# Optimization experiments

Hardware: AMD Instinct MI355X
Metric: run time of the kernel (lower is better)

The kernel has to match this reference:

```python
import jax, jax.numpy as jnp
import numpy as np

KERNELS = (4, 4, 8, 8, 8, 16, 16)
HEADS = (4, 4, 8, 8, 8, 16, 16)
PATCH = 2
EPS = 1e-5


def _layer_norm(x, w, b):
    mu = jnp.mean(x, axis=-1, keepdims=True)
    var = jnp.mean(jnp.square(x - mu), axis=-1, keepdims=True)
    return (x - mu) * jax.lax.rsqrt(var + EPS) * w + b


def _sliding_kernel_attention(x, w_qkv, k, heads):
    # x: (B, H, W, C) channels-last. Unfold -> per-window attention over the
    # k*k pixels (token dim = C) -> overlap-add fold (stride 1).
    B, H, W, C = x.shape
    Lh, Lw = H - k + 1, W - k + 1
    scale = (C // heads) ** -0.5
    ih = jnp.arange(Lh)[:, None] + jnp.arange(k)[None, :]   # (Lh, k)
    iw = jnp.arange(Lw)[:, None] + jnp.arange(k)[None, :]   # (Lw, k)
    pat = x[:, ih][:, :, :, iw]                             # (B, Lh, k, Lw, k, C)
    tok = pat.transpose(0, 1, 3, 2, 4, 5).reshape(B, Lh * Lw, k * k, C)
    qkv = jnp.einsum('blnc,dc->blnd', tok, w_qkv)           # (B, L, k*k, 3C)
    q, kk, v = jnp.split(qkv, 3, axis=-1)
    attn = jax.nn.softmax(jnp.einsum('blqc,blkc->blqk', q, kk) * scale, axis=-1)
    o = jnp.einsum('blqk,blkc->blqc', attn, v)              # (B, L, k*k, C)
    o = o.reshape(B, Lh, Lw, k, k, C).transpose(0, 1, 3, 2, 4, 5)  # (B,Lh,k,Lw,k,C)
    # overlap-add fold back to (B, H, W, C); duplicate indices accumulate
    return jnp.zeros_like(x).at[:, ih[:, :, None, None], iw[None, None, :, :], :].add(o)


def _block(x, ln1_w, ln1_b, w_qkv, ln2_w, ln2_b, w1, b1, w2, b2, k, heads):
    x = x + _sliding_kernel_attention(_layer_norm(x, ln1_w, ln1_b), w_qkv, k, heads)
    h = _layer_norm(x, ln2_w, ln2_b)
    h = jax.nn.gelu(h @ w1.T + b1, approximate=False)
    return x + (h @ w2.T + b2)


def _forward(x, patch_w, patch_b, row_emb, col_emb, cls_tok, ln1_w, ln1_b, qkv_w,
             ln2_w, ln2_b, mlp_w1, mlp_b1, mlp_w2, mlp_b2, cls_w, cls_b):
    # patch embed: conv k=stride=PATCH; output laid out channels-last (B, G, G, C)
    h = jax.lax.conv_general_dilated(
        x, patch_w, (PATCH, PATCH), 'VALID',
        dimension_numbers=('NCHW', 'OIHW', 'NHWC')) + patch_b
    B, G, _, C = h.shape
    # 2D positional embedding: row half + col half concatenated on channels
    pos = jnp.concatenate([
        jnp.broadcast_to(row_emb[:, None, :], (G, G, C // 2)),
        jnp.broadcast_to(col_emb[None, :, :], (G, G, C // 2))], axis=-1)
    h = h + pos
    # cls token: one extra row prepended along H (torch cat on dim=2)
    cls = jnp.broadcast_to(cls_tok, (B, 1, G, C))
    h = jnp.concatenate([cls, h], axis=1)                   # (B, G+1, G, C)
    for i in range(7):
        h = _block(h, ln1_w[i], ln1_b[i], qkv_w[i], ln2_w[i], ln2_b[i],
                   mlp_w1[i], mlp_b1[i], mlp_w2[i], mlp_b2[i],
                   KERNELS[i], HEADS[i])
    return h[:, 0, 0, :] @ cls_w.T + cls_b                  # (B, num_classes)


def setup_inputs() -> dict:
    key = jax.random.key(0)
    ks = jax.random.split(key, 8)
    B, C, G, NCLS, NB = 16, 256, 16, 1000, 7
    s = 0.02
    return {
        'x': jax.random.normal(ks[0], (B, 3, 32, 32), jnp.float32),
        'patch_w': jax.random.normal(ks[1], (C, 3, PATCH, PATCH), jnp.float32) * s,
        'patch_b': jnp.zeros((C,), jnp.float32),
        'row_emb': jax.random.normal(ks[2], (G, C // 2), jnp.float32) * s,
        'col_emb': jax.random.normal(ks[3], (G, C // 2), jnp.float32) * s,
        'cls_tok': jnp.zeros((C,), jnp.float32),
        'ln1_w': jnp.ones((NB, C), jnp.float32),
        'ln1_b': jnp.zeros((NB, C), jnp.float32),
        'qkv_w': jax.random.normal(ks[4], (NB, 3 * C, C), jnp.float32) * s,
        'ln2_w': jnp.ones((NB, C), jnp.float32),
        'ln2_b': jnp.zeros((NB, C), jnp.float32),
        'mlp_w1': jax.random.normal(ks[5], (NB, 2 * C, C), jnp.float32) * s,
        'mlp_b1': jnp.zeros((NB, 2 * C), jnp.float32),
        'mlp_w2': jax.random.normal(ks[6], (NB, C, 2 * C), jnp.float32) * s,
        'mlp_b2': jnp.zeros((NB, C), jnp.float32),
        'cls_w': jax.random.normal(ks[7], (NCLS, C), jnp.float32) * s,
        'cls_b': jnp.zeros((NCLS,), jnp.float32),
    }


def reference(x, patch_w, patch_b, row_emb, col_emb, cls_tok, ln1_w, ln1_b, qkv_w,
              ln2_w, ln2_b, mlp_w1, mlp_b1, mlp_w2, mlp_b2, cls_w, cls_b):
    return _forward(x, patch_w, patch_b, row_emb, col_emb, cls_tok, ln1_w, ln1_b,
                    qkv_w, ln2_w, ln2_b, mlp_w1, mlp_b1, mlp_w2, mlp_b2, cls_w, cls_b)
```

## Files before the change

kernel.cpp:

```cpp
#include <hip/hip_runtime.h>
#include <cmath>

#define NPIX 4352
#define C_DIM 256

typedef unsigned short ushort_t;
typedef unsigned int uint_t;
typedef float f32x4 __attribute__((ext_vector_type(4)));
typedef __bf16 bfx8 __attribute__((ext_vector_type(8)));

__device__ __forceinline__ ushort_t f2bf(float f) {
    uint_t u = __float_as_uint(f);
    u = (u + 0x7FFFu + ((u >> 16) & 1u)) >> 16;
    return (ushort_t)u;
}
__device__ __forceinline__ float bf2f(ushort_t b) {
    return __uint_as_float(((uint_t)b) << 16);
}
__device__ __forceinline__ float gelu_f(float v) {
    return 0.5f * v * (1.0f + erff(v * 0.70710678118654752f));
}

__global__ __launch_bounds__(256) void conv3_bf16(
    const float* __restrict__ a, ushort_t* __restrict__ oa, int na,
    const float* __restrict__ b, ushort_t* __restrict__ ob, int nb,
    const float* __restrict__ c, ushort_t* __restrict__ oc, int nc)
{
    int ntot = na + nb + nc;
    for (int i = blockIdx.x * 256 + threadIdx.x; i < ntot; i += gridDim.x * 256) {
        if (i < na)            oa[i] = f2bf(a[i]);
        else if (i < na + nb)  ob[i - na] = f2bf(b[i - na]);
        else                   oc[i - na - nb] = f2bf(c[i - na - nb]);
    }
}

__global__ __launch_bounds__(256) void patch_embed_ln(
    const float* __restrict__ x, const float* __restrict__ pw,
    const float* __restrict__ pb, const float* __restrict__ row_emb,
    const float* __restrict__ col_emb, const float* __restrict__ cls_tok,
    const float* __restrict__ lw, const float* __restrict__ lb,
    float* __restrict__ out, ushort_t* __restrict__ lnout)
{
    __shared__ float red[8];
    int p = blockIdx.x;
    int c = threadIdx.x;
    int b = p / 272;
    int rem = p - b * 272;
    int y = rem >> 4;
    int xw = rem & 15;
    float v;
    if (y == 0) {
        v = cls_tok[c];
    } else {
        int gr = y - 1, gc = xw;
        const float* xb = x + (size_t)b * 3 * 1024;
        const float* wc = pw + (size_t)c * 12;
        float acc = pb[c];
        #pragma unroll
        for (int ci = 0; ci < 3; ci++)
            #pragma unroll
            for (int ph = 0; ph < 2; ph++)
                #pragma unroll
                for (int pq = 0; pq < 2; pq++)
                    acc += xb[ci * 1024 + (2 * gr + ph) * 32 + (2 * gc + pq)]
                         * wc[(ci * 2 + ph) * 2 + pq];
        acc += (c < 128) ? row_emb[gr * 128 + c] : col_emb[gc * 128 + (c - 128)];
        v = acc;
    }
    out[(size_t)p * C_DIM + c] = v;
    float s = v;
    s += __shfl_down(s, 32); s += __shfl_down(s, 16); s += __shfl_down(s, 8);
    s += __shfl_down(s, 4);  s += __shfl_down(s, 2);  s += __shfl_down(s, 1);
    if ((c & 63) == 0) red[c >> 6] = s;
    __syncthreads();
    float mu = (red[0] + red[1] + red[2] + red[3]) * (1.0f / 256.0f);
    float d = v - mu;
    float s2 = d * d;
    s2 += __shfl_down(s2, 32); s2 += __shfl_down(s2, 16); s2 += __shfl_down(s2, 8);
    s2 += __shfl_down(s2, 4);  s2 += __shfl_down(s2, 2);  s2 += __shfl_down(s2, 1);
    if ((c & 63) == 0) red[4 + (c >> 6)] = s2;
    __syncthreads();
    float var = (red[4] + red[5] + red[6] + red[7]) * (1.0f / 256.0f);
    lnout[(size_t)p * C_DIM + c] = f2bf(d * rsqrtf(var + 1e-5f) * lw[c] + lb[c]);
}

__global__ __launch_bounds__(256) void layernorm_k(
    const float* __restrict__ in, const float* __restrict__ w,
    const float* __restrict__ b, ushort_t* __restrict__ out)
{
    __shared__ float red[8];
    int r = blockIdx.x, c = threadIdx.x;
    float v = in[(size_t)r * C_DIM + c];
    float s = v;
    s += __shfl_down(s, 32); s += __shfl_down(s, 16); s += __shfl_down(s, 8);
    s += __shfl_down(s, 4);  s += __shfl_down(s, 2);  s += __shfl_down(s, 1);
    if ((c & 63) == 0) red[c >> 6] = s;
    __syncthreads();
    float mu = (red[0] + red[1] + red[2] + red[3]) * (1.0f / 256.0f);
    float d = v - mu;
    float s2 = d * d;
    s2 += __shfl_down(s2, 32); s2 += __shfl_down(s2, 16); s2 += __shfl_down(s2, 8);
    s2 += __shfl_down(s2, 4);  s2 += __shfl_down(s2, 2);  s2 += __shfl_down(s2, 1);
    if ((c & 63) == 0) red[4 + (c >> 6)] = s2;
    __syncthreads();
    float var = (red[4] + red[5] + red[6] + red[7]) * (1.0f / 256.0f);
    out[(size_t)r * C_DIM + c] = f2bf(d * rsqrtf(var + 1e-5f) * w[c] + b[c]);
}

template <int BM, int BN, int MODE>
__global__ __launch_bounds__(256) void gemm_v2(
    const ushort_t* __restrict__ A, const ushort_t* __restrict__ B,
    const float* __restrict__ bias, const float* __restrict__ res,
    void* __restrict__ outp, ushort_t* __restrict__ vT, int K, int ldo)
{
    constexpr int MI = BM / 32, NJ = BN / 32;
    constexpr int AG = BM * 4, BG = BN * 4;
    constexpr int AU = AG / 256, BU = BG / 256;
    constexpr int HALF = (BM + BN) * 32;
    constexpr int STAGE_E = 2 * HALF;
    constexpr int BOUNCE_E = BM * (BN + 8);
    constexpr int SMEM_E = (STAGE_E > BOUNCE_E) ? STAGE_E : BOUNCE_E;
    __shared__ ushort_t sm[SMEM_E];

    int m0 = blockIdx.x * BM, n0 = blockIdx.y * BN;
    int t = threadIdx.x, lane = t & 63, wv = t >> 6;
    int l15 = lane & 15, lg = lane >> 4;
    int wr = wv >> 1, wc = wv & 1;

    const int nt = K / 32;
    f32x4 acc[MI][NJ] = {};
    uint4 ra[AU], rb[BU];

    #pragma unroll
    for (int u = 0; u < AU; u++) {
        int g = t + u * 256, row = g >> 2, p = g & 3;
        int ps = p ^ ((row >> 1) & 3);
        ra[u] = *(const uint4*)(A + (size_t)(m0 + row) * K + ps * 8);
    }
    #pragma unroll
    for (int u = 0; u < BU; u++) {
        int g = t + u * 256, col = g >> 2, p = g & 3;
        int ps = p ^ ((col >> 1) & 3);
        rb[u] = *(const uint4*)(B + (size_t)(n0 + col) * K + ps * 8);
    }
    #pragma unroll
    for (int u = 0; u < AU; u++) *(uint4*)(sm + (t + u * 256) * 8) = ra[u];
    #pragma unroll
    for (int u = 0; u < BU; u++) *(uint4*)(sm + BM * 32 + (t + u * 256) * 8) = rb[u];
    __syncthreads();

    for (int ks = 0; ks < nt; ks++) {
        int coff = (ks & 1) * HALF, noff = ((ks & 1) ^ 1) * HALF;
        if (ks + 1 < nt) {
            int k1 = (ks + 1) * 32;
            #pragma unroll
            for (int u = 0; u < AU; u++) {
                int g = t + u * 256, row = g >> 2, p = g & 3;
                int ps = p ^ ((row >> 1) & 3);
                ra[u] = *(const uint4*)(A + (size_t)(m0 + row) * K + k1 + ps * 8);
            }
            #pragma unroll
            for (int u = 0; u < BU; u++) {
                int g = t + u * 256, col = g >> 2, p = g & 3;
                int ps = p ^ ((col >> 1) & 3);
                rb[u] = *(const uint4*)(B + (size_t)(n0 + col) * K + k1 + ps * 8);
            }
        }
        bfx8 af[MI], bf[NJ];
        #pragma unroll
        for (int i = 0; i < MI; i++) {
            int row = wr * (BM / 2) + i * 16 + l15;
            af[i] = *(const bfx8*)(sm + coff + row * 32 + ((lg ^ ((row >> 1) & 3)) << 3));
        }
        #pragma unroll
        for (int j = 0; j < NJ; j++) {
            int col = wc * (BN / 2) + j * 16 + l15;
            bf[j] = *(const bfx8*)(sm + coff + BM * 32 + col * 32 + ((lg ^ ((col >> 1) & 3)) << 3));
        }
        #pragma unroll
        for (int i = 0; i < MI; i++)
            #pragma unroll
            for (int j = 0; j < NJ; j++)
                acc[i][j] = __builtin_amdgcn_mfma_f32_16x16x32_bf16(af[i], bf[j], acc[i][j], 0, 0, 0);
        if (ks + 1 < nt) {
            #pragma unroll
            for (int u = 0; u < AU; u++) *(uint4*)(sm + noff + (t + u * 256) * 8) = ra[u];
            #pragma unroll
            for (int u = 0; u < BU; u++) *(uint4*)(sm + noff + BM * 32 + (t + u * 256) * 8) = rb[u];
        }
        __syncthreads();
    }

    if (MODE == 0 && n0 >= 512) {
        #pragma unroll
        for (int i = 0; i < MI; i++) {
            int mb = m0 + wr * (BM / 2) + i * 16 + lg * 4;
            #pragma unroll
            for (int j = 0; j < NJ; j++) {
                int nv = n0 - 512 + wc * (BN / 2) + j * 16 + l15;
                ushort4 pk;
                pk.x = f2bf(acc[i][j][0]); pk.y = f2bf(acc[i][j][1]);
                pk.z = f2bf(acc[i][j][2]); pk.w = f2bf(acc[i][j][3]);
                *(ushort4*)&vT[(size_t)nv * NPIX + mb] = pk;
            }
        }
        return;
    }
    if (MODE == 3) {
        float* o = (float*)outp;
        #pragma unroll
        for (int i = 0; i < MI; i++) {
            #pragma unroll
            for (int j = 0; j < NJ; j++) {
                int col = n0 + wc * (BN / 2) + j * 16 + l15;
                float bz = bias[col];
                #pragma unroll
                for (int r = 0; r < 4; r++) {
                    int row = m0 + wr * (BM / 2) + i * 16 + lg * 4 + r;
                    o[(size_t)row * ldo + col] = acc[i][j][r] + bz + res[(size_t)row * ldo + col];
                }
            }
        }
        return;
    }
    __syncthreads();
    #pragma unroll
    for (int i = 0; i < MI; i++) {
        #pragma unroll
        for (int j = 0; j < NJ; j++) {
            int cl = wc * (BN / 2) + j * 16 + l15;
            float bz = (MODE == 2) ? bias[n0 + cl] : 0.0f;
            #pragma unroll
            for (int r = 0; r < 4; r++) {
                int rl = wr * (BM / 2) + i * 16 + lg * 4 + r;
                float v = acc[i][j][r];
                if (MODE == 2) v = gelu_f(v + bz);
                sm[rl * (BN + 8) + cl] = f2bf(v);
            }
        }
    }
    __syncthreads();
    ushort_t* ob = (ushort_t*)outp;
    #pragma unroll
    for (int e = 0; e < BM * BN; e += 2048) {
        int idx = e + t * 8;
        int rl = idx / BN, cl = idx % BN;
        uint4 v = *(const uint4*)(sm + rl * (BN + 8) + cl);
        *(uint4*)&ob[(size_t)(m0 + rl) * ldo + n0 + cl] = v;
    }
}

__device__ __forceinline__ uint2 ld_u4_align(const uint_t* drow, int e0) {
    int d0 = e0 >> 1;
    if (!(e0 & 1)) return make_uint2(drow[d0], drow[d0 + 1]);
    uint_t a = drow[d0], b = drow[d0 + 1], c = drow[d0 + 2];
    return make_uint2((a >> 16) | (b << 16), (b >> 16) | (c << 16));
}
__device__ __forceinline__ uint4 ld_u8_align(const uint_t* drow, int e0) {
    int d0 = e0 >> 1;
    if (!(e0 & 1)) return make_uint4(drow[d0], drow[d0 + 1], drow[d0 + 2], drow[d0 + 3]);
    uint_t a = drow[d0], b = drow[d0 + 1], c = drow[d0 + 2], d = drow[d0 + 3], e = drow[d0 + 4];
    return make_uint4((a >> 16) | (b << 16), (b >> 16) | (c << 16),
                      (c >> 16) | (d << 16), (d >> 16) | (e << 16));
}

template <int KK>
__global__ __launch_bounds__(256) void attn_v2(
    const ushort_t* __restrict__ qk, const ushort_t* __restrict__ vT,
    ushort_t* __restrict__ obuf, int w0, int nW, float scale)
{
    constexpr int T = KK * KK;
    constexpr int Lh = 18 - KK, Lw = 17 - KK, L = Lh * Lw;
    constexpr int NF   = 1;
    constexpr int NJ   = 8;
    constexpr int PSTR = 40;
    constexpr int KROWS = 32;
    constexpr int VROWS = 256;
    constexpr int EOFF = 2048;
    constexpr int ESTR = 128;

    __shared__ ushort_t Klds[KROWS * 256];
    __shared__ ushort_t Vlds[VROWS * 64];
    __shared__ ushort_t Plds[4][16 * PSTR];

    int t = threadIdx.x, lane = t & 63, wv = t >> 6;
    int l15 = lane & 15, lg = lane >> 4;

    int wrel = blockIdx.x * 2 + (wv & 1);
    int wloc = wv & 1, chalf = wv >> 1, qbase = 0;
    if (wrel >= nW) wrel = nW - 1;

    int pbs[2];
    #pragma unroll
    for (int w = 0; w < 2; w++) {
        int wi = blockIdx.x * 2 + w;
        if (wi >= nW) wi = nW - 1;
        wi += w0;
        int b = wi / L, lrem = wi % L;
        pbs[w] = b * 272 + (lrem / Lw) * 16 + (lrem % Lw);
    }

    int qtok = qbase + l15;
    int qpix = pbs[wloc] + ((qtok >> 2) << 4) + (qtok & 3);
    bfx8 qf[8];
    #pragma unroll
    for (int cs = 0; cs < 8; cs++)
        qf[cs] = *(const bfx8*)(qk + (size_t)qpix * 512 + cs * 32 + lg * 8);

    f32x4 o[NJ] = {};
    float lsum[4] = {0.f, 0.f, 0.f, 0.f};

    for (int g = t; g < KROWS * 32; g += 256) {
        int row = g >> 5, cg = g & 31;
        int pix = pbs[row >> 4] + (((row & 15) >> 2) << 4) + (row & 3);
        uint4 v = *(const uint4*)(qk + (size_t)pix * 512 + 256 + cg * 8);
        *(uint4*)(Klds + row * 256 + ((cg ^ (row & 7)) << 3)) = v;
    }
    for (int g = t; g < VROWS * 8; g += 256) {
        int cr = g >> 3, c16 = g & 7;
        const uint_t* drow = (const uint_t*)(vT + (size_t)cr * NPIX);
        uint4 v;
        int w = c16 >> 2, sub = c16 & 3;
        if (sub < 2) {
            int pix0 = pbs[w] + (sub << 5);
            uint2 a  = ld_u4_align(drow, pix0);
            uint2 b2 = ld_u4_align(drow, pix0 + 16);
            v = make_uint4(a.x, a.y, b2.x, b2.y);
        } else v = make_uint4(0, 0, 0, 0);
        *(uint4*)(Vlds + cr * 64 + ((c16 ^ (cr & 7)) << 3)) = v;
    }
    __syncthreads();
    f32x4 s[NF];
    #pragma unroll
    for (int j = 0; j < NF; j++) s[j] = f32x4{0.f, 0.f, 0.f, 0.f};
    #pragma unroll
    for (int cs = 0; cs < 8; cs++) {
        int krow = (wloc << 4) + l15;
        bfx8 kf = *(const bfx8*)(Klds + krow * 256 + ((((cs << 2) + lg) ^ (krow & 7)) << 3));
        s[0] = __builtin_amdgcn_mfma_f32_16x16x32_bf16(qf[cs], kf, s[0], 0, 0, 0);
    }
    float p[NF][4];
    #pragma unroll
    for (int r = 0; r < 4; r++) {
        float mx = s[0][r];
        mx = fmaxf(mx, __shfl_xor(mx, 1));
        mx = fmaxf(mx, __shfl_xor(mx, 2));
        mx = fmaxf(mx, __shfl_xor(mx, 4));
        mx = fmaxf(mx, __shfl_xor(mx, 8));
        float ps = 0.f;
        p[0][r] = __expf(scale * (s[0][r] - mx));
        ps += p[0][r];
        ps += __shfl_xor(ps, 1);
        ps += __shfl_xor(ps, 2);
        ps += __shfl_xor(ps, 4);
        ps += __shfl_xor(ps, 8);
        lsum[r] = ps;
    }
    ushort_t* Pw = Plds[wv];
    #pragma unroll
    for (int r = 0; r < 4; r++) {
        Pw[(lg * 4 + r) * PSTR + l15] = f2bf(p[0][r]);
        Pw[(lg * 4 + r) * PSTR + 16 + l15] = 0;
    }
    asm volatile("s_waitcnt lgkmcnt(0)" ::: "memory");
    __builtin_amdgcn_sched_barrier(0);
    {
        bfx8 pf = *(const bfx8*)(Pw + l15 * PSTR + (lg << 3));
        #pragma unroll
        for (int j = 0; j < NJ; j++) {
            int cr = chalf * 128 + (j << 4) + l15;
            int c16 = ((wloc << 2) + lg) ^ (cr & 7);
            bfx8 vf = *(const bfx8*)(Vlds + cr * 64 + (c16 << 3));
            o[j] = __builtin_amdgcn_mfma_f32_16x16x32_bf16(pf, vf, o[j], 0, 0, 0);
        }
    }
    asm volatile("s_waitcnt lgkmcnt(0)" ::: "memory");
    __syncthreads();
    float inv[4];
    #pragma unroll
    for (int r = 0; r < 4; r++) inv[r] = 1.0f / lsum[r];
    ushort_t* Ep = Klds + wv * EOFF;
    #pragma unroll
    for (int j = 0; j < NJ; j++)
        #pragma unroll
        for (int r = 0; r < 4; r++)
            Ep[(lg * 4 + r) * ESTR + (j << 4) + l15] = f2bf(o[j][r] * inv[r]);
    asm volatile("s_waitcnt lgkmcnt(0)" ::: "memory");
    __builtin_amdgcn_sched_barrier(0);
    size_t gb = ((size_t)wrel * T + qbase) * C_DIM + chalf * 128;
    #pragma unroll
    for (int i = 0; i < 4; i++) {
        int off = i * 512 + lane * 8;
        int row = off >> 7, col = off & 127;
        uint4 v = *(const uint4*)(Ep + row * ESTR + col);
        *(uint4*)(obuf + gb + (size_t)row * C_DIM + col) = v;
    }
}

__global__ __launch_bounds__(256) void attn_v3(
    const ushort_t* __restrict__ qk, const ushort_t* __restrict__ vT,
    ushort_t* __restrict__ obuf, int w0, float scale)
{
    __shared__ ushort_t SH[32768];
    const int Lw = 9, L = 90;
    int t = threadIdx.x, lane = t & 63, wv = t >> 6;
    int l15 = lane & 15, lg = lane >> 4;
    int wrel = blockIdx.x;
    int widx = w0 + wrel;
    int b = widx / L, lrem = widx % L;
    int pbase = b * 272 + (lrem / Lw) * 16 + (lrem % Lw);
    int qbase = wv * 16;

    int qtok = qbase + l15;
    int qpix = pbase + ((qtok >> 3) << 4) + (qtok & 7);
    bfx8 qf[8];
    #pragma unroll
    for (int cs = 0; cs < 8; cs++)
        qf[cs] = *(const bfx8*)(qk + (size_t)qpix * 512 + cs * 32 + lg * 8);

    for (int g = t; g < 64 * 32; g += 256) {
        int row = g >> 5, cg = g & 31;
        int pix = pbase + ((row >> 3) << 4) + (row & 7);
        uint4 v = *(const uint4*)(qk + (size_t)pix * 512 + 256 + cg * 8);
        *(uint4*)(SH + row * 256 + ((cg ^ (row & 7)) << 3)) = v;
    }
    for (int g = t; g < 256 * 8; g += 256) {
        int cr = g >> 3, c16 = g & 7;
        const uint_t* drow = (const uint_t*)(vT + (size_t)cr * NPIX);
        uint4 v = ld_u8_align(drow, pbase + (c16 << 4));
        *(uint4*)(SH + 16384 + cr * 64 + ((c16 ^ (cr & 7)) << 3)) = v;
    }
    __syncthreads();

    f32x4 s[4];
    #pragma unroll
    for (int j = 0; j < 4; j++) s[j] = f32x4{0.f, 0.f, 0.f, 0.f};
    #pragma unroll
    for (int cs = 0; cs < 8; cs++) {
        #pragma unroll
        for (int j = 0; j < 4; j++) {
            int krow = (j << 4) + l15;
            bfx8 kf = *(const bfx8*)(SH + krow * 256 + ((((cs << 2) + lg) ^ (krow & 7)) << 3));
            s[j] = __builtin_amdgcn_mfma_f32_16x16x32_bf16(qf[cs], kf, s[j], 0, 0, 0);
        }
    }
    float p[4][4], lsum[4];
    #pragma unroll
    for (int r = 0; r < 4; r++) {
        float mx = s[0][r];
        #pragma unroll
        for (int j = 1; j < 4; j++) mx = fmaxf(mx, s[j][r]);
        mx = fmaxf(mx, __shfl_xor(mx, 1));
        mx = fmaxf(mx, __shfl_xor(mx, 2));
        mx = fmaxf(mx, __shfl_xor(mx, 4));
        mx = fmaxf(mx, __shfl_xor(mx, 8));
        float ps = 0.f;
        #pragma unroll
        for (int j = 0; j < 4; j++) {
            p[j][r] = __expf(scale * (s[j][r] - mx));
            ps += p[j][r];
        }
        ps += __shfl_xor(ps, 1);
        ps += __shfl_xor(ps, 2);
        ps += __shfl_xor(ps, 4);
        ps += __shfl_xor(ps, 8);
        lsum[r] = ps;
    }
    __syncthreads();
    ushort_t* Pw = SH + wv * 1088;
    #pragma unroll
    for (int j = 0; j < 4; j++)
        #pragma unroll
        for (int r = 0; r < 4; r++)
            Pw[(lg * 4 + r) * 68 + (j << 4) + l15] = f2bf(p[j][r]);
    asm volatile("s_waitcnt lgkmcnt(0)" ::: "memory");
    __builtin_amdgcn_sched_barrier(0);
    f32x4 o[16] = {};
    #pragma unroll
    for (int kt = 0; kt < 2; kt++) {
        bfx8 pf = *(const bfx8*)(Pw + l15 * 68 + (kt << 5) + (lg << 3));
        #pragma unroll
        for (int j = 0; j < 16; j++) {
            int cr = (j << 4) + l15;
            int c16 = ((kt << 2) + lg) ^ (cr & 7);
            bfx8 vf = *(const bfx8*)(SH + 16384 + cr * 64 + (c16 << 3));
            o[j] = __builtin_amdgcn_mfma_f32_16x16x32_bf16(pf, vf, o[j], 0, 0, 0);
        }
    }
    asm volatile("s_waitcnt lgkmcnt(0)" ::: "memory");
    __syncthreads();
    float inv[4];
    #pragma unroll
    for (int r = 0; r < 4; r++) inv[r] = 1.0f / lsum[r];
    ushort_t* Ep = SH + wv * 4224;
    #pragma unroll
    for (int j = 0; j < 16; j++)
        #pragma unroll
        for (int r = 0; r < 4; r++)
            Ep[(lg * 4 + r) * 260 + (j << 4) + l15] = f2bf(o[j][r] * inv[r]);
    asm volatile("s_waitcnt lgkmcnt(0)" ::: "memory");
    __builtin_amdgcn_sched_barrier(0);
    size_t gb = ((size_t)wrel * 64 + qbase) * C_DIM;
    #pragma unroll
    for (int i = 0; i < 8; i++) {
        int off = i * 512 + lane * 8;
        int row = off >> 8, col = off & 255;
        uint4 v = *(const uint4*)(Ep + row * 260 + col);
        *(uint4*)(obuf + gb + off) = v;
    }
}

template <int PASS>
__global__ __launch_bounds__(256) void gemm_seq(
    const ushort_t* __restrict__ A, const ushort_t* __restrict__ B,
    const float* __restrict__ linv, void* __restrict__ outp)
{
    __shared__ ushort_t sm[8192];
    int m0 = blockIdx.x * 64, n0 = blockIdx.y * 64;
    int seq = blockIdx.z;
    int pbase = (seq >> 1) * 272 + (seq & 1) * 16;
    int t = threadIdx.x, lane = t & 63, wv = t >> 6;
    int l15 = lane & 15, lg = lane >> 4;
    int wr = wv >> 1, wc = wv & 1;

    f32x4 acc[2][2] = {};
    uint4 ra, rb;

    int g_row = t >> 2, g_p = t & 3;
    int g_ps = g_p ^ ((g_row >> 1) & 3);

    const ushort_t* Asrc;
    const ushort_t* Bsrc;
    if (PASS == 0) {
        Asrc = A + (size_t)(pbase + m0 + g_row) * 512 + g_ps * 8;
        Bsrc = B + (size_t)(pbase + n0 + g_row) * 512 + 256 + g_ps * 8;
    } else {
        Asrc = A + (size_t)seq * 65536 + (size_t)(m0 + g_row) * 256 + g_ps * 8;
        Bsrc = B + (size_t)(n0 + g_row) * NPIX + pbase + g_ps * 8;
    }

    ra = *(const uint4*)(Asrc);
    rb = *(const uint4*)(Bsrc);
    *(uint4*)(sm + t * 8) = ra;
    *(uint4*)(sm + 2048 + t * 8) = rb;
    __syncthreads();

    for (int ks = 0; ks < 8; ks++) {
        int coff = (ks & 1) * 4096, noff = ((ks & 1) ^ 1) * 4096;
        if (ks + 1 < 8) {
            int k1 = (ks + 1) * 32;
            ra = *(const uint4*)(Asrc + k1);
            rb = *(const uint4*)(Bsrc + k1);
        }
        bfx8 af[2], bf[2];
        #pragma unroll
        for (int i = 0; i < 2; i++) {
            int row = wr * 32 + i * 16 + l15;
            af[i] = *(const bfx8*)(sm + coff + row * 32 + ((lg ^ ((row >> 1) & 3)) << 3));
        }
        #pragma unroll
        for (int j = 0; j < 2; j++) {
            int col = wc * 32 + j * 16 + l15;
            bf[j] = *(const bfx8*)(sm + coff + 2048 + col * 32 + ((lg ^ ((col >> 1) & 3)) << 3));
        }
        #pragma unroll
        for (int i = 0; i < 2; i++)
            #pragma unroll
            for (int j = 0; j < 2; j++)
                acc[i][j] = __builtin_amdgcn_mfma_f32_16x16x32_bf16(af[i], bf[j], acc[i][j], 0, 0, 0);
        if (ks + 1 < 8) {
            *(uint4*)(sm + noff + t * 8) = ra;
            *(uint4*)(sm + noff + 2048 + t * 8) = rb;
        }
        __syncthreads();
    }

    if (PASS == 0) {
        float* S = (float*)outp + (size_t)seq * 65536;
        #pragma unroll
        for (int i = 0; i < 2; i++) {
            #pragma unroll
            for (int j = 0; j < 2; j++) {
                int col = n0 + wc * 32 + j * 16 + l15;
                #pragma unroll
                for (int r = 0; r < 4; r++) {
                    int row = m0 + wr * 32 + i * 16 + lg * 4 + r;
                    S[(size_t)row * 256 + col] = acc[i][j][r];
                }
            }
        }
        return;
    }
    ushort_t* ob = (ushort_t*)outp;
    #pragma unroll
    for (int i = 0; i < 2; i++) {
        #pragma unroll
        for (int j = 0; j < 2; j++) {
            int cl = wc * 32 + j * 16 + l15;
            #pragma unroll
            for (int r = 0; r < 4; r++) {
                int rl = wr * 32 + i * 16 + lg * 4 + r;
                float v = acc[i][j][r] * linv[seq * 256 + m0 + rl];
                sm[rl * 72 + cl] = f2bf(v);
            }
        }
    }
    __syncthreads();
    #pragma unroll
    for (int e = 0; e < 4096; e += 2048) {
        int idx = e + t * 8;
        int rl = idx >> 6, cl = idx & 63;
        uint4 v = *(const uint4*)(sm + rl * 72 + cl);
        *(uint4*)&ob[(size_t)seq * 65536 + (size_t)(m0 + rl) * 256 + n0 + cl] = v;
    }
}

__global__ __launch_bounds__(256) void rowsm(
    const float* __restrict__ sbuf, ushort_t* __restrict__ pbuf,
    float* __restrict__ linv, float scale)
{
    __shared__ float red[8];
    int r = blockIdx.x, t = threadIdx.x;
    float s = sbuf[(size_t)r * 256 + t];
    float m = s;
    m = fmaxf(m, __shfl_down(m, 32)); m = fmaxf(m, __shfl_down(m, 16));
    m = fmaxf(m, __shfl_down(m, 8));  m = fmaxf(m, __shfl_down(m, 4));
    m = fmaxf(m, __shfl_down(m, 2));  m = fmaxf(m, __shfl_down(m, 1));
    if ((t & 63) == 0) red[t >> 6] = m;
    __syncthreads();
    m = fmaxf(fmaxf(red[0], red[1]), fmaxf(red[2], red[3]));
    float p = __expf(scale * (s - m));
    float ps = p;
    ps += __shfl_down(ps, 32); ps += __shfl_down(ps, 16); ps += __shfl_down(ps, 8);
    ps += __shfl_down(ps, 4);  ps += __shfl_down(ps, 2);  ps += __shfl_down(ps, 1);
    if ((t & 63) == 0) red[4 + (t >> 6)] = ps;
    __syncthreads();
    float sum = red[4] + red[5] + red[6] + red[7];
    pbuf[(size_t)r * 256 + t] = f2bf(p);
    if (t == 0) linv[r] = 1.0f / sum;
}

__global__ __launch_bounds__(256) void fold_ln(
    const ushort_t* __restrict__ obuf, const float* __restrict__ xin,
    float* __restrict__ y, const float* __restrict__ lw,
    const float* __restrict__ lb, ushort_t* __restrict__ lnout, int do_ln,
    int k, int Lh, int Lw, int w0, int w1)
{
    __shared__ float red[8];
    int p = blockIdx.x;
    int c = threadIdx.x;
    int b = p / 272;
    int rem = p - b * 272;
    int yy = rem >> 4, xx = rem & 15;
    int L = Lh * Lw;
    int T = k * k;
    float acc = xin ? xin[(size_t)p * C_DIM + c] : y[(size_t)p * C_DIM + c];
    int lh0 = max(0, yy - k + 1), lh1 = min(Lh - 1, yy);
    int lw0 = max(0, xx - k + 1), lw1 = min(Lw - 1, xx);
    for (int lh = lh0; lh <= lh1; lh++) {
        for (int lw = lw0; lw <= lw1; lw++) {
            int widx = b * L + lh * Lw + lw;
            if (widx < w0 || widx >= w1) continue;
            int n = (yy - lh) * k + (xx - lw);
            acc += bf2f(obuf[((size_t)(widx - w0) * T + n) * C_DIM + c]);
        }
    }
    y[(size_t)p * C_DIM + c] = acc;
    if (!do_ln) return;
    float s = acc;
    s += __shfl_down(s, 32); s += __shfl_down(s, 16); s += __shfl_down(s, 8);
    s += __shfl_down(s, 4);  s += __shfl_down(s, 2);  s += __shfl_down(s, 1);
    if ((c & 63) == 0) red[c >> 6] = s;
    __syncthreads();
    float mu = (red[0] + red[1] + red[2] + red[3]) * (1.0f / 256.0f);
    float d = acc - mu;
    float s2 = d * d;
    s2 += __shfl_down(s2, 32); s2 += __shfl_down(s2, 16); s2 += __shfl_down(s2, 8);
    s2 += __shfl_down(s2, 4);  s2 += __shfl_down(s2, 2);  s2 += __shfl_down(s2, 1);
    if ((c & 63) == 0) red[4 + (c >> 6)] = s2;
    __syncthreads();
    float var = (red[4] + red[5] + red[6] + red[7]) * (1.0f / 256.0f);
    lnout[(size_t)p * C_DIM + c] = f2bf(d * rsqrtf(var + 1e-5f) * lw[c] + lb[c]);
}

__global__ __launch_bounds__(256) void classifier_k(
    const float* __restrict__ h, const float* __restrict__ cw,
    const float* __restrict__ cb, float* __restrict__ out)
{
    __shared__ float hrow[256];
    int b = blockIdx.x;
    int n = blockIdx.y * 256 + threadIdx.x;
    hrow[threadIdx.x] = h[(size_t)b * 272 * C_DIM + threadIdx.x];
    __syncthreads();
    if (n < 1000) {
        float acc = cb[n];
        const float* wr = cw + (size_t)n * C_DIM;
        for (int c = 0; c < 256; c++) acc += hrow[c] * wr[c];
        out[(size_t)b * 1000 + n] = acc;
    }
}

extern "C" void kernel_launch(void* const* d_in, const int* in_sizes, int n_in,
                              void* d_out, int out_size, void* d_ws, size_t ws_size,
                              hipStream_t stream)
{
    const float* x       = (const float*)d_in[0];
    const float* patch_w = (const float*)d_in[1];
    const float* patch_b = (const float*)d_in[2];
    const float* row_emb = (const float*)d_in[3];
    const float* col_emb = (const float*)d_in[4];
    const float* cls_tok = (const float*)d_in[5];
    const float* ln1_w   = (const float*)d_in[6];
    const float* ln1_b   = (const float*)d_in[7];
    const float* qkv_w   = (const float*)d_in[8];
    const float* ln2_w   = (const float*)d_in[9];
    const float* ln2_b   = (const float*)d_in[10];
    const float* mlp_w1  = (const float*)d_in[11];
    const float* mlp_b1  = (const float*)d_in[12];
    const float* mlp_w2  = (const float*)d_in[13];
    const float* mlp_b2  = (const float*)d_in[14];
    const float* cls_w   = (const float*)d_in[15];
    const float* cls_b   = (const float*)d_in[16];
    float* out = (float*)d_out;

    float* xb0  = (float*)d_ws;
    float* xb1  = xb0 + (size_t)NPIX * 256;
    ushort_t* lnb = (ushort_t*)(xb1 + (size_t)NPIX * 256);
    ushort_t* qkb = lnb + (size_t)NPIX * 256;
    ushort_t* vT  = qkb + (size_t)NPIX * 512;
    ushort_t* h1  = vT + (size_t)256 * NPIX;
    ushort_t* wq  = h1 + (size_t)NPIX * 512;
    ushort_t* w1b = wq + (size_t)7 * 768 * 256;
    ushort_t* w2b = w1b + (size_t)7 * 512 * 256;
    float* sbuf   = (float*)(w2b + (size_t)7 * 256 * 512);
    ushort_t* pbuf = (ushort_t*)(sbuf + (size_t)32 * 65536);
    float* linv   = (float*)(pbuf + (size_t)32 * 65536);
    ushort_t* obuf = (ushort_t*)(linv + 8192);
    size_t obuf_off_bytes = (size_t)((char*)obuf - (char*)d_ws);
    size_t obuf_cap_e = (ws_size > obuf_off_bytes + 64)
                        ? (ws_size - obuf_off_bytes - 64) / 2 : 0;

    conv3_bf16<<<1024, 256, 0, stream>>>(qkv_w, wq, 7 * 768 * 256,
                                         mlp_w1, w1b, 7 * 512 * 256,
                                         mlp_w2, w2b, 7 * 256 * 512);

    patch_embed_ln<<<NPIX, 256, 0, stream>>>(x, patch_w, patch_b, row_emb,
                                             col_emb, cls_tok, ln1_w, ln1_b,
                                             xb0, lnb);

    const int KS[7] = {4, 4, 8, 8, 8, 16, 16};
    float* xcur = xb0;
    float* ybuf = xb1;

    for (int i = 0; i < 7; i++) {
        int k = KS[i];
        int Lh = 18 - k, Lw = 17 - k, L = Lh * Lw, T = k * k;
        float scale = 1.0f / std::sqrt((float)(256 / k));

        if (i > 0)
            layernorm_k<<<NPIX, 256, 0, stream>>>(xcur, ln1_w + i * 256,
                                                  ln1_b + i * 256, lnb);
        gemm_v2<128, 128, 0><<<dim3(NPIX / 128, 6), 256, 0, stream>>>(
            lnb, wq + (size_t)i * 768 * 256, nullptr, nullptr, qkb, vT, 256, 512);

        if (k == 16) {
            gemm_seq<0><<<dim3(4, 4, 32), 256, 0, stream>>>(qkb, qkb, nullptr, sbuf);
            rowsm<<<8192, 256, 0, stream>>>(sbuf, pbuf, linv, scale);
            gemm_seq<1><<<dim3(4, 4, 32), 256, 0, stream>>>(pbuf, vT, linv, obuf);
            fold_ln<<<NPIX, 256, 0, stream>>>(obuf, xcur, ybuf,
                                              ln2_w + i * 256, ln2_b + i * 256,
                                              lnb, 1, k, Lh, Lw, 0, 32);
        } else {
            int totalW = 16 * L;
            size_t perW = (size_t)T * C_DIM;
            int maxW = (int)((obuf_cap_e / perW) < (size_t)totalW
                             ? (obuf_cap_e / perW) : (size_t)totalW);
            if (maxW < 2) maxW = 2;
            if (k == 4) maxW &= ~1;
            for (int w0 = 0; w0 < totalW; w0 += maxW) {
                int nW = totalW - w0 < maxW ? totalW - w0 : maxW;
                if (k == 4)
                    attn_v2<4><<<(nW + 1) / 2, 256, 0, stream>>>(qkb, vT, obuf, w0, nW, scale);
                else
                    attn_v3<<<nW, 256, 0, stream>>>(qkb, vT, obuf, w0, scale);
                int last = (w0 + nW >= totalW);
                fold_ln<<<NPIX, 256, 0, stream>>>(obuf, (w0 == 0) ? xcur : nullptr,
                                                  ybuf, ln2_w + i * 256, ln2_b + i * 256,
                                                  lnb, last, k, Lh, Lw, w0, w0 + nW);
            }
        }

        gemm_v2<64, 128, 2><<<dim3(NPIX / 64, 4), 256, 0, stream>>>(
            lnb, w1b + (size_t)i * 512 * 256, mlp_b1 + i * 512, nullptr, h1, nullptr, 256, 512);
        gemm_v2<64, 64, 3><<<dim3(NPIX / 64, 4), 256, 0, stream>>>(
            h1, w2b + (size_t)i * 256 * 512, mlp_b2 + i * 256, ybuf, xcur, nullptr, 512, 256);
    }

    classifier_k<<<dim3(16, 4), 256, 0, stream>>>(xcur, cls_w, cls_b, out);
}
```

Before: 725.6 us.

## Split overlap-add fold into row-sum and column-sum passes for small kernels

For k=4 and k=8 layers, when the whole attention output fits in the workspace, attention runs in a single launch instead of chunked windows. The fold then runs in two stages: foldA sums each window row's outputs along the horizontal direction into per-row partial sums, and foldB adds the vertical contributions, the residual and the layer norm. This replaces the per-pixel gather over k*k overlapping windows with separable summation, cutting redundant bf16 reads and removing the chunk loop. The cost is an extra fp32 rowsum buffer that shares space with sbuf, and obuf moves to a fixed offset after it.

Result: faster. 644.2 us (-11.2%).

```diff
diff --git a/kernel.cpp b/kernel.cpp
--- a/kernel.cpp
+++ b/kernel.cpp
@@ -638,6 +638,66 @@
     float sum = red[4] + red[5] + red[6] + red[7];
     pbuf[(size_t)r * 256 + t] = f2bf(p);
     if (t == 0) linv[r] = 1.0f / sum;
+}
+
+template <int K>
+__global__ __launch_bounds__(256) void foldA(
+    const ushort_t* __restrict__ obuf, float* __restrict__ rowsum)
+{
+    constexpr int Lh = 18 - K, Lw = 17 - K, L = Lh * Lw, T = K * K;
+    int c = threadIdx.x;
+    int bid = blockIdx.x;
+    int dy = bid % K;
+    int blh = bid / K;
+    int lh = blh % Lh;
+    int b = blh / Lh;
+    float acc[16];
+    #pragma unroll
+    for (int x = 0; x < 16; x++) acc[x] = 0.f;
+    const ushort_t* base = obuf + ((size_t)(b * L + lh * Lw) * T + dy * K) * C_DIM + c;
+    #pragma unroll
+    for (int lw = 0; lw < Lw; lw++)
+        #pragma unroll
+        for (int dx = 0; dx < K; dx++)
+            acc[lw + dx] += bf2f(base[((size_t)lw * T + dx) * C_DIM]);
+    float* orow = rowsum + (size_t)bid * 16 * C_DIM + c;
+    #pragma unroll
+    for (int x = 0; x < 16; x++) orow[(size_t)x * C_DIM] = acc[x];
+}
+
+template <int K>
+__global__ __launch_bounds__(256) void foldB(
+    const float* __restrict__ rowsum, const float* __restrict__ xin,
+    float* __restrict__ y, const float* __restrict__ lw_,
+    const float* __restrict__ lb_, ushort_t* __restrict__ lnout)
+{
+    constexpr int Lh = 18 - K;
+    __shared__ float red[8];
+    int p = blockIdx.x, c = threadIdx.x;
+    int b = p / 272, rem = p - b * 272;
+    int yy = rem >> 4, xx = rem & 15;
+    float acc = xin[(size_t)p * C_DIM + c];
+    #pragma unroll
+    for (int dy = 0; dy < K; dy++) {
+        int lh = yy - dy;
+        if (lh >= 0 && lh < Lh)
+            acc += rowsum[(((size_t)(b * Lh + lh) * K + dy) * 16 + xx) * C_DIM + c];
+    }
+    y[(size_t)p * C_DIM + c] = acc;
+    float s = acc;
+    s += __shfl_down(s, 32); s += __shfl_down(s, 16); s += __shfl_down(s, 8);
+    s += __shfl_down(s, 4);  s += __shfl_down(s, 2);  s += __shfl_down(s, 1);
+    if ((c & 63) == 0) red[c >> 6] = s;
+    __syncthreads();
+    float mu = (red[0] + red[1] + red[2] + red[3]) * (1.0f / 256.0f);
+    float d = acc - mu;
+    float s2 = d * d;
+    s2 += __shfl_down(s2, 32); s2 += __shfl_down(s2, 16); s2 += __shfl_down(s2, 8);
+    s2 += __shfl_down(s2, 4);  s2 += __shfl_down(s2, 2);  s2 += __shfl_down(s2, 1);
+    if ((c & 63) == 0) red[4 + (c >> 6)] = s2;
+    __syncthreads();
+    float var = (red[4] + red[5] + red[6] + red[7]) * (1.0f / 256.0f);
+    lnout[(size_t)p * C_DIM + c] = f2bf(d * rsqrtf(var + 1e-5f) * lw_[c] + lb_[c]);
 }
 
 __global__ __launch_bounds__(256) void fold_ln(
@@ -732,10 +792,12 @@
     ushort_t* wq  = h1 + (size_t)NPIX * 512;
     ushort_t* w1b = wq + (size_t)7 * 768 * 256;
     ushort_t* w2b = w1b + (size_t)7 * 512 * 256;
-    float* sbuf   = (float*)(w2b + (size_t)7 * 256 * 512);
+    float* scratch = (float*)(w2b + (size_t)7 * 256 * 512);
+    float* rowsum  = scratch;
+    float* sbuf    = scratch;
     ushort_t* pbuf = (ushort_t*)(sbuf + (size_t)32 * 65536);
-    float* linv   = (float*)(pbuf + (size_t)32 * 65536);
-    ushort_t* obuf = (ushort_t*)(linv + 8192);
+    float* linv    = (float*)(pbuf + (size_t)32 * 65536);
+    ushort_t* obuf = (ushort_t*)(rowsum + 5242880);
     size_t obuf_off_bytes = (size_t)((char*)obuf - (char*)d_ws);
     size_t obuf_cap_e = (ws_size > obuf_off_bytes + 64)
                         ? (ws_size - obuf_off_bytes - 64) / 2 : 0;
@@ -763,6 +825,7 @@
         gemm_v2<128, 128, 0><<<dim3(NPIX / 128, 6), 256, 0, stream>>>(
             lnb, wq + (size_t)i * 768 * 256, nullptr, nullptr, qkb, vT, 256, 512);
 
+        int totalW = 16 * L;
         if (k == 16) {
             gemm_seq<0><<<dim3(4, 4, 32), 256, 0, stream>>>(qkb, qkb, nullptr, sbuf);
             rowsm<<<8192, 256, 0, stream>>>(sbuf, pbuf, linv, scale);
@@ -770,11 +833,21 @@
             fold_ln<<<NPIX, 256, 0, stream>>>(obuf, xcur, ybuf,
                                               ln2_w + i * 256, ln2_b + i * 256,
                                               lnb, 1, k, Lh, Lw, 0, 32);
+        } else if ((size_t)totalW * T * C_DIM <= obuf_cap_e) {
+            if (k == 4) {
+                attn_v2<4><<<(totalW + 1) / 2, 256, 0, stream>>>(qkb, vT, obuf, 0, totalW, scale);
+                foldA<4><<<16 * 14 * 4, 256, 0, stream>>>(obuf, rowsum);
+                foldB<4><<<NPIX, 256, 0, stream>>>(rowsum, xcur, ybuf,
+                                                   ln2_w + i * 256, ln2_b + i * 256, lnb);
+            } else {
+                attn_v3<<<totalW, 256, 0, stream>>>(qkb, vT, obuf, 0, scale);
+                foldA<8><<<16 * 10 * 8, 256, 0, stream>>>(obuf, rowsum);
+                foldB<8><<<NPIX, 256, 0, stream>>>(rowsum, xcur, ybuf,
+                                                   ln2_w + i * 256, ln2_b + i * 256, lnb);
+            }
         } else {
-            int totalW = 16 * L;
             size_t perW = (size_t)T * C_DIM;
-            int maxW = (int)((obuf_cap_e / perW) < (size_t)totalW
-                             ? (obuf_cap_e / perW) : (size_t)totalW);
+            int maxW = (int)(obuf_cap_e / perW);
             if (maxW < 2) maxW = 2;
             if (k == 4) maxW &= ~1;
             for (int w0 = 0; w0 < totalW; w0 += maxW) {
```
